# Optimization experiments

Measured on AMD Instinct MI355X. Metric: run time of the kernel, lower is better.

The kernel has to match this reference:

```python
import jax, jax.numpy as jnp
import numpy as np

B, H, S, D = 1, 16, 4096, 64


def setup_inputs() -> dict:
    key = jax.random.key(0)
    kq, kk, kv = jax.random.split(key, 3)
    Q = jax.random.normal(kq, (B, H, S, D), dtype=jnp.float32)
    K = jax.random.normal(kk, (B, H, S, D), dtype=jnp.float32)
    V = jax.random.normal(kv, (B, H, S, D), dtype=jnp.float32)
    # causal mask, broadcast over batch/heads: True = attend
    mask = jnp.tril(jnp.ones((S, S), dtype=bool))[None, None, :, :]
    return {"Q": Q, "K": K, "V": V, "mask": mask}


def reference(Q, K, V, mask):
    d_k = Q.shape[-1]
    scale = 1.0 / jnp.sqrt(jnp.asarray(d_k, dtype=Q.dtype))
    # [..., q, k] scores; mask==False positions set to -inf before softmax
    scores = jnp.einsum('...qd,...kd->...qk', Q, K) * scale
    scores = jnp.where(mask, scores, jnp.asarray(-jnp.inf, dtype=scores.dtype))
    attn = jax.nn.softmax(scores, axis=-1)
    return jnp.einsum('...qk,...kd->...qd', attn, V)
```

## Files before the change

### kernel.cpp

```cpp
#include <hip/hip_runtime.h>
#include <hip/hip_bf16.h>

typedef __attribute__((ext_vector_type(8))) short short8;
typedef __attribute__((ext_vector_type(4))) short s4v;
typedef __attribute__((ext_vector_type(4))) int   int4v;
typedef __attribute__((ext_vector_type(4))) float floatx4;

#define MFMA16(A,B,C) __builtin_amdgcn_mfma_f32_16x16x32_bf16(A,B,C,0,0,0)

__device__ __forceinline__ short bf16bits(float x) {
    __hip_bfloat16 h = __float2bfloat16(x);
    return *(short*)&h;
}
__device__ __forceinline__ short8 cvt8(const float* p) {
    floatx4 a = *(const floatx4*)p;
    floatx4 b = *(const floatx4*)(p + 4);
    short8 r;
    r[0]=bf16bits(a.x); r[1]=bf16bits(a.y); r[2]=bf16bits(a.z); r[3]=bf16bits(a.w);
    r[4]=bf16bits(b.x); r[5]=bf16bits(b.y); r[6]=bf16bits(b.z); r[7]=bf16bits(b.w);
    return r;
}
__device__ __forceinline__ short8 cvt8s(const float* p) {
    constexpr float SCL2 = 0.125f * 1.44269504088896f;
    floatx4 a = *(const floatx4*)p;
    floatx4 b = *(const floatx4*)(p + 4);
    a *= SCL2; b *= SCL2;
    short8 r;
    r[0]=bf16bits(a.x); r[1]=bf16bits(a.y); r[2]=bf16bits(a.z); r[3]=bf16bits(a.w);
    r[4]=bf16bits(b.x); r[5]=bf16bits(b.y); r[6]=bf16bits(b.z); r[7]=bf16bits(b.w);
    return r;
}
__device__ __forceinline__ int pk2(float lo, float hi) {
    int r;
    asm("v_cvt_pk_bf16_f32 %0, %1, %2" : "=v"(r) : "v"(lo), "v"(hi));
    return r;
}

__global__ __launch_bounds__(256) void prep(const float* __restrict__ V,
                                            short* __restrict__ VT,
                                            const float* __restrict__ K,
                                            short* __restrict__ K16, int doK)
{
    __shared__ short tile[64 * 65];
    const int t  = threadIdx.x;
    const int h  = blockIdx.x >> 6;
    const int s0 = (blockIdx.x & 63) << 6;
    const float* src = V + ((size_t)h * 4096 + s0) * 64;
    const int r = t >> 4, dq = (t & 15) * 4;
#pragma unroll
    for (int pass = 0; pass < 4; ++pass) {
        const int s = pass * 16 + r;
        floatx4 f = *(const floatx4*)(src + s * 64 + dq);
        short* w = tile + s * 65 + dq;
        w[0] = bf16bits(f.x); w[1] = bf16bits(f.y);
        w[2] = bf16bits(f.z); w[3] = bf16bits(f.w);
    }
    __syncthreads();
    const int d = t >> 2, sc = (t & 3) * 16;
    short8 a, b;
#pragma unroll
    for (int j = 0; j < 8; ++j) a[j] = tile[(sc + j) * 65 + d];
#pragma unroll
    for (int j = 0; j < 8; ++j) b[j] = tile[(sc + 8 + j) * 65 + d];
    short* dst = VT + ((size_t)h * 64 + d) * 4096 + s0 + sc;
    *(short8*)dst       = a;
    *(short8*)(dst + 8) = b;
    if (doK) {
        const size_t base = (size_t)blockIdx.x * 4096 + (size_t)t * 16;
        *(short8*)(K16 + base)     = cvt8(K + base);
        *(short8*)(K16 + base + 8) = cvt8(K + base + 8);
    }
}

__global__ __attribute__((amdgpu_waves_per_eu(4, 4))) __launch_bounds__(256)
void attn_split(const float* __restrict__ Qg, const short* __restrict__ K16g,
                const short* __restrict__ VTg, float* __restrict__ Og,
                float* __restrict__ partO, float* __restrict__ partL)
{
    constexpr int S = 4096, D = 64;

    __shared__ __align__(16) short lK[8192];
    __shared__ __align__(16) short lV[8192];

    const int tid = threadIdx.x;
    const int wv  = tid >> 6;
    const int ln  = tid & 63;
    const int ll  = ln & 15;
    const int qd  = ln >> 4;
    const int qhalf = wv & 1;
    const int khalf = wv >> 1;

    const int bid = blockIdx.x;
    const int h = bid / 95;
    const int u = bid % 95;
    int qblk, ks, ke, slot;
    if (u < 62) {
        qblk = 63 - (u >> 1);
        const int part = u & 1;
        const int T = qblk + 1, Th = T >> 1;
        ks = part ? Th : 0;
        ke = part ? T : Th;
        slot = (h * 31 + (qblk - 33)) * 2 + part;
    } else {
        qblk = 94 - u;
        ks = 0; ke = qblk + 1;
        slot = -1;
    }
    const int qb   = qblk << 6;
    const int qrow = qb + (qhalf << 5);

    const float* Qh  = Qg  + (size_t)h * S * D;
    const short* K16 = K16g + (size_t)h * S * D;
    const short* Vt  = VTg + (size_t)h * 64 * S;

    short8 qA0, qA1, qB0, qB1;
    {
        const float* qp = Qh + (qrow + ll) * D + qd * 8;
        qA0 = cvt8s(qp);       qA1 = cvt8s(qp + 32);
        const float* qp2 = qp + 16 * D;
        qB0 = cvt8s(qp2);      qB1 = cvt8s(qp2 + 32);
    }

    floatx4 oA[4], oB[4], olA, olB;
#pragma unroll
    for (int dt = 0; dt < 4; ++dt) { oA[dt] = (floatx4){0.f,0.f,0.f,0.f}; oB[dt] = oA[dt]; }
    olA = (floatx4){0.f,0.f,0.f,0.f};
    olB = olA;

    short8 ones;
#pragma unroll
    for (int j = 0; j < 8; ++j) ones[j] = (short)0x3F80;

    const int kkey = tid >> 3, kd8 = tid & 7;
    const int koct = kd8 & 3;
    short* kdst = lK + ((kkey >> 4) * 2 + (kd8 >> 2)) * 512
                     + ((((kkey & 15) | (koct << 4)) ^ (koct * 5)) * 8);
    const short* ksrc6 = K16 + kkey * 64 + kd8 * 8;
    const int vd = tid >> 2, voct = tid & 3;
    short* vdst = lV + (vd >> 4) * 512
                     + ((((vd & 15) | (voct << 4)) ^ (voct * 5)) * 8);
    const short* vsrc = Vt + (size_t)vd * S + voct * 8;
    const int rblk = ((ll | (qd << 4)) ^ (qd * 5));

    const int wv_end = qrow + 32;

    auto mkpf = [&](floatx4 sc0, floatx4 sc1, int qgrp, int kvh) -> short8 {
        float p0[4], p1[4];
#pragma unroll
        for (int r = 0; r < 4; ++r) { p0[r] = exp2f(sc0[r]); p1[r] = exp2f(sc1[r]); }
        if (kvh + 31 > qgrp) {
            const int qg = qgrp + ll;
            const int k0 = kvh + qd * 4, k1 = k0 + 16;
#pragma unroll
            for (int r = 0; r < 4; ++r) {
                if (k0 + r > qg) p0[r] = 0.f;
                if (k1 + r > qg) p1[r] = 0.f;
            }
        }
        int w0 = pk2(p0[0], p0[1]);
        int w1 = pk2(p0[2], p0[3]);
        int w2 = pk2(p1[0], p1[1]);
        int w3 = pk2(p1[2], p1[3]);
        asm("v_permlane32_swap_b32 %0, %1" : "+v"(w0), "+v"(w2));
        asm("v_permlane32_swap_b32 %0, %1" : "+v"(w1), "+v"(w3));
        asm("v_permlane16_swap_b32 %0, %1" : "+v"(w0), "+v"(w2));
        asm("v_permlane16_swap_b32 %0, %1" : "+v"(w1), "+v"(w3));
        int4v pv = {w0, w1, w2, w3};
        return *(short8*)&pv;
    };

    short8 kp0 = *(const short8*)(ksrc6 + ks * 64 * 64);
    short8 kp1 = *(const short8*)(ksrc6 + (ks * 64 + 32) * 64);
    short8 vp0 = *(const short8*)(vsrc + ks * 64);
    short8 vp1 = *(const short8*)(vsrc + ks * 64 + 32);

    int bo = 0;
    for (int t = ks; t <= ke; ++t) {
        __syncthreads();
        if (t < ke) {
            *(short8*)(kdst + bo)        = kp0;
            *(short8*)(kdst + bo + 2048) = kp1;
            *(short8*)(vdst + bo)        = vp0;
            *(short8*)(vdst + bo + 2048) = vp1;
            if (t + 1 < ke) {
                const int nk = (t + 1) << 6;
                kp0 = *(const short8*)(ksrc6 + (size_t)nk * 64);
                kp1 = *(const short8*)(ksrc6 + (size_t)(nk + 32) * 64);
                vp0 = *(const short8*)(vsrc + nk);
                vp1 = *(const short8*)(vsrc + nk + 32);
            }
        }
        if (t > ks) {
            const int kv  = (t - 1) << 6;
            const int kvw = kv + (khalf << 5);
            if (kvw < wv_end) {
                const int ro = (bo ^ 4096) + (khalf << 11);
                const short* Kb = lK + ro;
                const short* Vb = lV + ro;
                floatx4 zz = (floatx4){0.f,0.f,0.f,0.f};
                floatx4 sA0=zz, sA1=zz, sB0=zz, sB1=zz;
                short8 kf;
                __builtin_amdgcn_s_setprio(1);
                kf = ((const short8*)(Kb +    0))[rblk]; sA0 = MFMA16(kf, qA0, sA0); sB0 = MFMA16(kf, qB0, sB0);
                kf = ((const short8*)(Kb +  512))[rblk]; sA0 = MFMA16(kf, qA1, sA0); sB0 = MFMA16(kf, qB1, sB0);
                kf = ((const short8*)(Kb + 1024))[rblk]; sA1 = MFMA16(kf, qA0, sA1); sB1 = MFMA16(kf, qB0, sB1);
                kf = ((const short8*)(Kb + 1536))[rblk]; sA1 = MFMA16(kf, qA1, sA1); sB1 = MFMA16(kf, qB1, sB1);
                __builtin_amdgcn_s_setprio(0);

                short8 pfA = mkpf(sA0, sA1, qrow,      kvw);
                short8 pfB = mkpf(sB0, sB1, qrow + 16, kvw);
                __builtin_amdgcn_s_setprio(1);
#pragma unroll
                for (int dt = 0; dt < 4; ++dt) {
                    short8 vf = ((const short8*)(Vb + dt * 512))[rblk];
                    oA[dt] = MFMA16(pfA, vf, oA[dt]);
                    oB[dt] = MFMA16(pfB, vf, oB[dt]);
                }
                olA = MFMA16(pfA, ones, olA);
                olB = MFMA16(pfB, ones, olB);
                __builtin_amdgcn_s_setprio(0);
            }
        }
        bo ^= 4096;
    }

    __syncthreads();
    float* sAod = (float*)lK;
    float* sBod = (float*)lV;
    const int mbase = ((qhalf << 6) + ln) * 20;
    if (khalf == 1) {
#pragma unroll
        for (int dt = 0; dt < 4; ++dt)
#pragma unroll
            for (int r = 0; r < 4; ++r) {
                sAod[mbase + dt * 4 + r] = oA[dt][r];
                sBod[mbase + dt * 4 + r] = oB[dt][r];
            }
#pragma unroll
        for (int r = 0; r < 4; ++r) {
            sAod[mbase + 16 + r] = olA[r];
            sBod[mbase + 16 + r] = olB[r];
        }
    }
    __syncthreads();
    if (khalf == 0) {
#pragma unroll
        for (int dt = 0; dt < 4; ++dt)
#pragma unroll
            for (int r = 0; r < 4; ++r) {
                oA[dt][r] += sAod[mbase + dt * 4 + r];
                oB[dt][r] += sBod[mbase + dt * 4 + r];
            }
#pragma unroll
        for (int r = 0; r < 4; ++r) {
            olA[r] += sAod[mbase + 16 + r];
            olB[r] += sBod[mbase + 16 + r];
        }
        if (slot < 0) {
#pragma unroll
            for (int r = 0; r < 4; ++r) {
                const float rl = 1.f / fmaxf(olA[r], 1e-37f);
                const int q = qrow + qd * 4 + r;
                float* op = Og + ((size_t)h * S + q) * D + ll;
#pragma unroll
                for (int dt = 0; dt < 4; ++dt)
                    op[dt * 16] = oA[dt][r] * rl;
            }
#pragma unroll
            for (int r = 0; r < 4; ++r) {
                const float rl = 1.f / fmaxf(olB[r], 1e-37f);
                const int q = qrow + 16 + qd * 4 + r;
                float* op = Og + ((size_t)h * S + q) * D + ll;
#pragma unroll
                for (int dt = 0; dt < 4; ++dt)
                    op[dt * 16] = oB[dt][r] * rl;
            }
        } else {
            float* po = partO + (size_t)slot * 4096;
            float* pl = partL + (size_t)slot * 64;
#pragma unroll
            for (int r = 0; r < 4; ++r) {
                const int row = (qhalf << 5) + qd * 4 + r;
                float* op = po + row * 64 + ll;
#pragma unroll
                for (int dt = 0; dt < 4; ++dt)
                    op[dt * 16] = oA[dt][r];
                if (ll == 0) pl[row] = olA[r];
            }
#pragma unroll
            for (int r = 0; r < 4; ++r) {
                const int row = (qhalf << 5) + 16 + qd * 4 + r;
                float* op = po + row * 64 + ll;
#pragma unroll
                for (int dt = 0; dt < 4; ++dt)
                    op[dt * 16] = oB[dt][r];
                if (ll == 0) pl[row] = olB[r];
            }
        }
    }
}

__global__ __launch_bounds__(256) void merge_split(const float* __restrict__ pO,
                                                   const float* __restrict__ pL,
                                                   float* __restrict__ Og)
{
    const int bid = blockIdx.x;
    const int h  = bid / 31;
    const int qb = (33 + bid % 31) << 6;
    const size_t b0 = (size_t)(bid * 2) * 4096;
    const int t = threadIdx.x;
#pragma unroll
    for (int k = 0; k < 4; ++k) {
        const int idx = t * 4 + k * 1024;
        const int row = idx >> 6;
        floatx4 a = *(const floatx4*)(pO + b0 + idx);
        floatx4 b = *(const floatx4*)(pO + b0 + 4096 + idx);
        const float l = pL[bid * 128 + row] + pL[bid * 128 + 64 + row];
        const float rl = 1.f / fmaxf(l, 1e-37f);
        floatx4 o;
        o.x = (a.x + b.x) * rl; o.y = (a.y + b.y) * rl;
        o.z = (a.z + b.z) * rl; o.w = (a.w + b.w) * rl;
        *(floatx4*)(Og + ((size_t)h * 4096 + qb + row) * 64 + (idx & 63)) = o;
    }
}

template<bool KB16>
__global__ __attribute__((amdgpu_waves_per_eu(4, 4))) __launch_bounds__(256)
void attn_fast(const float* __restrict__ Qg, const float* __restrict__ Kg,
               const short* __restrict__ K16g, const short* __restrict__ VTg,
               float* __restrict__ Og)
{
    constexpr int S = 4096, D = 64;
    __shared__ __align__(16) short lK[8192];
    __shared__ __align__(16) short lV[8192];
    const int tid = threadIdx.x;
    const int wv  = tid >> 6;
    const int ln  = tid & 63;
    const int ll  = ln & 15;
    const int qd  = ln >> 4;
    const int qhalf = wv & 1;
    const int khalf = wv >> 1;
    const int c = blockIdx.x & 255;
    const int s = blockIdx.x >> 8;
    const int h = c & 15;
    const int x = c >> 4;
    const int qblk = (s == 0) ? (63 - x) : (s == 1) ? (32 + x) : (s == 2) ? (31 - x) : x;
    const int qb   = qblk << 6;
    const int qrow = qb + (qhalf << 5);
    const float* Qh  = Qg  + (size_t)h * S * D;
    const float* Kf  = Kg  + (size_t)h * S * D;
    const short* K16 = K16g + (size_t)h * S * D;
    const short* Vt  = VTg + (size_t)h * 64 * S;
    short8 qA0, qA1, qB0, qB1;
    {
        const float* qp = Qh + (qrow + ll) * D + qd * 8;
        qA0 = cvt8s(qp);       qA1 = cvt8s(qp + 32);
        const float* qp2 = qp + 16 * D;
        qB0 = cvt8s(qp2);      qB1 = cvt8s(qp2 + 32);
    }
    floatx4 oA[4], oB[4], olA, olB;
#pragma unroll
    for (int dt = 0; dt < 4; ++dt) { oA[dt] = (floatx4){0.f,0.f,0.f,0.f}; oB[dt] = oA[dt]; }
    olA = (floatx4){0.f,0.f,0.f,0.f};
    olB = olA;
    short8 ones;
#pragma unroll
    for (int j = 0; j < 8; ++j) ones[j] = (short)0x3F80;
    const int kkey = tid >> 3, kd8 = tid & 7;
    const int koct = kd8 & 3;
    short* kdst = lK + ((kkey >> 4) * 2 + (kd8 >> 2)) * 512
                     + ((((kkey & 15) | (koct << 4)) ^ (koct * 5)) * 8);
    const float* ksrcf = Kf  + kkey * 64 + kd8 * 8;
    const short* ksrc6 = K16 + kkey * 64 + kd8 * 8;
    const int vd = tid >> 2, voct = tid & 3;
    short* vdst = lV + (vd >> 4) * 512
                     + ((((vd & 15) | (voct << 4)) ^ (voct * 5)) * 8);
    const short* vsrc = Vt + (size_t)vd * S + voct * 8;
    const int rblk = ((ll | (qd << 4)) ^ (qd * 5));
    const int kv_end = qb + 64;
    const int wv_end = qrow + 32;
    auto ldK = [&](int kv) -> short8 {
        return KB16 ? *(const short8*)(ksrc6 + kv * 64) : cvt8(ksrcf + kv * 64);
    };
    auto mkpf = [&](floatx4 sc0, floatx4 sc1, int qgrp, int kvh) -> short8 {
        float p0[4], p1[4];
#pragma unroll
        for (int r = 0; r < 4; ++r) { p0[r] = exp2f(sc0[r]); p1[r] = exp2f(sc1[r]); }
        if (kvh + 31 > qgrp) {
            const int qg = qgrp + ll;
            const int k0 = kvh + qd * 4, k1 = k0 + 16;
#pragma unroll
            for (int r = 0; r < 4; ++r) {
                if (k0 + r > qg) p0[r] = 0.f;
                if (k1 + r > qg) p1[r] = 0.f;
            }
        }
        int w0 = pk2(p0[0], p0[1]);
        int w1 = pk2(p0[2], p0[3]);
        int w2 = pk2(p1[0], p1[1]);
        int w3 = pk2(p1[2], p1[3]);
        asm("v_permlane32_swap_b32 %0, %1" : "+v"(w0), "+v"(w2));
        asm("v_permlane32_swap_b32 %0, %1" : "+v"(w1), "+v"(w3));
        asm("v_permlane16_swap_b32 %0, %1" : "+v"(w0), "+v"(w2));
        asm("v_permlane16_swap_b32 %0, %1" : "+v"(w1), "+v"(w3));
        int4v pv = {w0, w1, w2, w3};
        return *(short8*)&pv;
    };
    short8 kp0 = ldK(0),  kp1 = ldK(32);
    short8 vp0 = *(const short8*)(vsrc);
    short8 vp1 = *(const short8*)(vsrc + 32);
    const int ntiles = kv_end >> 6;
    int bo = 0;
    for (int t = 0; t <= ntiles; ++t) {
        __syncthreads();
        if (t < ntiles) {
            *(short8*)(kdst + bo)        = kp0;
            *(short8*)(kdst + bo + 2048) = kp1;
            *(short8*)(vdst + bo)        = vp0;
            *(short8*)(vdst + bo + 2048) = vp1;
            const int nk = (t + 1) << 6;
            if (nk < kv_end) {
                kp0 = ldK(nk);
                kp1 = ldK(nk + 32);
                vp0 = *(const short8*)(vsrc + nk);
                vp1 = *(const short8*)(vsrc + nk + 32);
            }
        }
        if (t > 0) {
            const int kv  = (t - 1) << 6;
            const int kvw = kv + (khalf << 5);
            if (kvw < wv_end) {
                const int ro = (bo ^ 4096) + (khalf << 11);
                const short* Kb = lK + ro;
                const short* Vb = lV + ro;
                floatx4 zz = (floatx4){0.f,0.f,0.f,0.f};
                floatx4 sA0=zz, sA1=zz, sB0=zz, sB1=zz;
                short8 kf;
                __builtin_amdgcn_s_setprio(1);
                kf = ((const short8*)(Kb +    0))[rblk]; sA0 = MFMA16(kf, qA0, sA0); sB0 = MFMA16(kf, qB0, sB0);
                kf = ((const short8*)(Kb +  512))[rblk]; sA0 = MFMA16(kf, qA1, sA0); sB0 = MFMA16(kf, qB1, sB0);
                kf = ((const short8*)(Kb + 1024))[rblk]; sA1 = MFMA16(kf, qA0, sA1); sB1 = MFMA16(kf, qB0, sB1);
                kf = ((const short8*)(Kb + 1536))[rblk]; sA1 = MFMA16(kf, qA1, sA1); sB1 = MFMA16(kf, qB1, sB1);
                __builtin_amdgcn_s_setprio(0);
                short8 pfA = mkpf(sA0, sA1, qrow,      kvw);
                short8 pfB = mkpf(sB0, sB1, qrow + 16, kvw);
                __builtin_amdgcn_s_setprio(1);
#pragma unroll
                for (int dt = 0; dt < 4; ++dt) {
                    short8 vf = ((const short8*)(Vb + dt * 512))[rblk];
                    oA[dt] = MFMA16(pfA, vf, oA[dt]);
                    oB[dt] = MFMA16(pfB, vf, oB[dt]);
                }
                olA = MFMA16(pfA, ones, olA);
                olB = MFMA16(pfB, ones, olB);
                __builtin_amdgcn_s_setprio(0);
            }
        }
        bo ^= 4096;
    }
    __syncthreads();
    float* sAod = (float*)lK;
    float* sBod = (float*)lV;
    const int mbase = ((qhalf << 6) + ln) * 20;
    if (khalf == 1) {
#pragma unroll
        for (int dt = 0; dt < 4; ++dt)
#pragma unroll
            for (int r = 0; r < 4; ++r) {
                sAod[mbase + dt * 4 + r] = oA[dt][r];
                sBod[mbase + dt * 4 + r] = oB[dt][r];
            }
#pragma unroll
        for (int r = 0; r < 4; ++r) {
            sAod[mbase + 16 + r] = olA[r];
            sBod[mbase + 16 + r] = olB[r];
        }
    }
    __syncthreads();
    if (khalf == 0) {
#pragma unroll
        for (int dt = 0; dt < 4; ++dt)
#pragma unroll
            for (int r = 0; r < 4; ++r) {
                oA[dt][r] += sAod[mbase + dt * 4 + r];
                oB[dt][r] += sBod[mbase + dt * 4 + r];
            }
#pragma unroll
        for (int r = 0; r < 4; ++r) {
            olA[r] += sAod[mbase + 16 + r];
            olB[r] += sBod[mbase + 16 + r];
        }
#pragma unroll
        for (int r = 0; r < 4; ++r) {
            const float rl = 1.f / fmaxf(olA[r], 1e-37f);
            const int q = qrow + qd * 4 + r;
            float* op = Og + ((size_t)h * S + q) * D + ll;
#pragma unroll
            for (int dt = 0; dt < 4; ++dt)
                op[dt * 16] = oA[dt][r] * rl;
        }
#pragma unroll
        for (int r = 0; r < 4; ++r) {
            const float rl = 1.f / fmaxf(olB[r], 1e-37f);
            const int q = qrow + 16 + qd * 4 + r;
            float* op = Og + ((size_t)h * S + q) * D + ll;
#pragma unroll
            for (int dt = 0; dt < 4; ++dt)
                op[dt * 16] = oB[dt][r] * rl;
        }
    }
}

__global__ __launch_bounds__(256, 4)
void attn_legacy(const float* __restrict__ Qg, const float* __restrict__ Kg,
                 const float* __restrict__ Vg, float* __restrict__ Og)
{
    constexpr int S = 4096, D = 64;
    constexpr float SCL2 = 0.125f * 1.44269504088896f;
    constexpr float NEG  = -1.0e30f;
    __shared__ __align__(16) short lK[2048];
    __shared__ __align__(16) short lV[2048];
    __shared__ __align__(16) short lP[2048];
    const int tid = threadIdx.x, wv = tid >> 6, ln = tid & 63, ll = ln & 15, qd = ln >> 4;
    const int bid = blockIdx.x, h = bid & 15, qblk = 63 - (bid >> 4), qb = qblk << 6;
    const float* Qh = Qg + (size_t)h * S * D;
    const float* Kh = Kg + (size_t)h * S * D;
    const float* Vh = Vg + (size_t)h * S * D;
    const int qrow = qb + wv * 16;
    short8 qf0, qf1;
    { const float* qp = Qh + (qrow + ll) * D + qd * 8; qf0 = cvt8(qp); qf1 = cvt8(qp + 32); }
    floatx4 o[4]; float mi[4], li[4];
#pragma unroll
    for (int dt = 0; dt < 4; ++dt) o[dt] = (floatx4){0.f,0.f,0.f,0.f};
#pragma unroll
    for (int r = 0; r < 4; ++r) { mi[r] = NEG; li[r] = 0.f; }
    const int k_st = tid >> 3, dbase = (tid & 7) * 8;
    const int sq = (dbase >> 3) & 3, sks = dbase >> 5;
    const int kw_slot = (((k_st >> 4) * 2 + sks) * 64)
                      + (((sq << 4) | (k_st & 15)) ^ (sq | (sks << 2)));
    const int kr0 = ln ^ qd, kr1 = ln ^ (qd | 4), vbit3 = (ln >> 3) & 1;
    const int kv_end = qb + 64, wv_end = qrow + 16;
    for (int kv = 0; kv < kv_end; kv += 32) {
        __syncthreads();
        {
            short8 kval = cvt8(Kh + (kv + k_st) * D + dbase);
            ((short8*)lK)[kw_slot] = kval;
            short8 vval = cvt8(Vh + (kv + k_st) * D + dbase);
            const int vq = (k_st >> 3) << 4, vj = k_st & 7;
#pragma unroll
            for (int i = 0; i < 8; ++i) {
                int d = dbase + i, dt = d >> 4, l2 = d & 15;
                int lp = (vq | l2) ^ (((l2 >> 3) & 1) | (dt << 1));
                lV[dt * 512 + lp * 8 + vj] = vval[i];
            }
        }
        __syncthreads();
        if (kv < wv_end) {
            floatx4 sc0 = (floatx4){0.f,0.f,0.f,0.f}, sc1 = sc0; short8 kf;
            kf = ((const short8*)lK)[0*64+kr0]; sc0 = MFMA16(qf0, kf, sc0);
            kf = ((const short8*)lK)[1*64+kr1]; sc0 = MFMA16(qf1, kf, sc0);
            kf = ((const short8*)lK)[2*64+kr0]; sc1 = MFMA16(qf0, kf, sc1);
            kf = ((const short8*)lK)[3*64+kr1]; sc1 = MFMA16(qf1, kf, sc1);
            float p0[4], p1[4]; const int qg = qrow + qd * 4;
#pragma unroll
            for (int r = 0; r < 4; ++r) { p0[r] = sc0[r]*SCL2; p1[r] = sc1[r]*SCL2; }
            if (kv + 31 > qrow) {
                const int k0 = kv + ll, k1 = kv + 16 + ll;
#pragma unroll
                for (int r = 0; r < 4; ++r) {
                    if (k0 > qg + r) p0[r] = NEG;
                    if (k1 > qg + r) p1[r] = NEG;
                }
            }
#pragma unroll
            for (int r = 0; r < 4; ++r) {
                float mx = fmaxf(p0[r], p1[r]);
                mx = fmaxf(mx, __shfl_xor(mx,1)); mx = fmaxf(mx, __shfl_xor(mx,2));
                mx = fmaxf(mx, __shfl_xor(mx,4)); mx = fmaxf(mx, __shfl_xor(mx,8));
                const float nm = fmaxf(mi[r], mx);
                const float a = exp2f(mi[r] - nm); mi[r] = nm;
                p0[r] = exp2f(p0[r] - nm); p1[r] = exp2f(p1[r] - nm);
                float ps = p0[r] + p1[r];
                ps += __shfl_xor(ps,1); ps += __shfl_xor(ps,2);
                ps += __shfl_xor(ps,4); ps += __shfl_xor(ps,8);
                li[r] = li[r] * a + ps;
#pragma unroll
                for (int dt = 0; dt < 4; ++dt) o[dt][r] *= a;
            }
            {
                const int pbase = wv * 512 + (ll & 7);
                const int dl0 = ((ll >> 3) << 4) + qd * 4;
#pragma unroll
                for (int r = 0; r < 4; ++r) {
                    lP[pbase + (dl0 + r) * 8]      = bf16bits(p0[r]);
                    lP[pbase + (dl0 + 32 + r) * 8] = bf16bits(p1[r]);
                }
            }
            __threadfence_block();
            short8 pf = ((const short8*)lP)[wv * 64 + ln];
#pragma unroll
            for (int dt = 0; dt < 4; ++dt) {
                short8 vf = ((const short8*)lV)[dt * 64 + (ln ^ (vbit3 | (dt << 1)))];
                o[dt] = MFMA16(pf, vf, o[dt]);
            }
        }
    }
#pragma unroll
    for (int r = 0; r < 4; ++r) {
        const float rl = 1.f / fmaxf(li[r], 1e-30f);
        const int q = qrow + qd * 4 + r;
        float* op = Og + ((size_t)h * S + q) * D + ll;
#pragma unroll
        for (int dt = 0; dt < 4; ++dt) op[dt * 16] = o[dt][r] * rl;
    }
}

extern "C" void kernel_launch(void* const* d_in, const int* in_sizes, int n_in,
                              void* d_out, int out_size, void* d_ws, size_t ws_size,
                              hipStream_t stream) {
    const float* Q = (const float*)d_in[0];
    const float* K = (const float*)d_in[1];
    const float* V = (const float*)d_in[2];
    float* O = (float*)d_out;
    const size_t elems  = (size_t)16 * 4096 * 64;
    const size_t oneBuf = elems * sizeof(short);
    const size_t partOB = (size_t)992 * 4096 * sizeof(float);
    const size_t partLB = (size_t)992 * 64 * sizeof(float);
    if (ws_size >= 2 * oneBuf + partOB + partLB) {
        short* VT  = (short*)d_ws;
        short* K16 = (short*)d_ws + elems;
        float* pO  = (float*)((char*)d_ws + 2 * oneBuf);
        float* pL  = pO + (size_t)992 * 4096;
        prep<<<dim3(1024), dim3(256), 0, stream>>>(V, VT, K, K16, 1);
        attn_split<<<dim3(1520), dim3(256), 0, stream>>>(Q, K16, VT, O, pO, pL);
        merge_split<<<dim3(496), dim3(256), 0, stream>>>(pO, pL, O);
    } else if (ws_size >= 2 * oneBuf) {
        short* VT  = (short*)d_ws;
        short* K16 = (short*)d_ws + elems;
        prep<<<dim3(1024), dim3(256), 0, stream>>>(V, VT, K, K16, 1);
        attn_fast<true><<<dim3(1024), dim3(256), 0, stream>>>(Q, K, K16, VT, O);
    } else if (ws_size >= oneBuf) {
        short* VT = (short*)d_ws;
        prep<<<dim3(1024), dim3(256), 0, stream>>>(V, VT, K, VT, 0);
        attn_fast<false><<<dim3(1024), dim3(256), 0, stream>>>(Q, K, nullptr, VT, O);
    } else {
        attn_legacy<<<dim3(1024), dim3(256), 0, stream>>>(Q, K, V, O);
    }
}
```

Baseline: 203.5 us.

## Rebalance causal split-K work into paired equal-length block segments

```diff
diff --git a/kernel.cpp b/kernel.cpp
--- a/kernel.cpp
+++ b/kernel.cpp
@@ -72,10 +72,10 @@
     }
 }
 
-__global__ __attribute__((amdgpu_waves_per_eu(4, 4))) __launch_bounds__(256)
-void attn_split(const float* __restrict__ Qg, const short* __restrict__ K16g,
-                const short* __restrict__ VTg, float* __restrict__ Og,
-                float* __restrict__ partO, float* __restrict__ partL)
+__global__ __attribute__((amdgpu_waves_per_eu(4, 8))) __launch_bounds__(256)
+void attn_pair(const float* __restrict__ Qg, const short* __restrict__ K16g,
+               const short* __restrict__ VTg, float* __restrict__ Og,
+               float* __restrict__ partO, float* __restrict__ partL)
 {
     constexpr int S = 4096, D = 64;
 
@@ -90,46 +90,14 @@
     const int qhalf = wv & 1;
     const int khalf = wv >> 1;
 
-    const int bid = blockIdx.x;
-    const int h = bid / 95;
-    const int u = bid % 95;
-    int qblk, ks, ke, slot;
-    if (u < 62) {
-        qblk = 63 - (u >> 1);
-        const int part = u & 1;
-        const int T = qblk + 1, Th = T >> 1;
-        ks = part ? Th : 0;
-        ke = part ? T : Th;
-        slot = (h * 31 + (qblk - 33)) * 2 + part;
-    } else {
-        qblk = 94 - u;
-        ks = 0; ke = qblk + 1;
-        slot = -1;
-    }
-    const int qb   = qblk << 6;
-    const int qrow = qb + (qhalf << 5);
+    const int bid  = blockIdx.x;
+    const int h    = bid & 15;
+    const int x    = (bid >> 4) & 31;
+    const int role = bid >> 9;
 
     const float* Qh  = Qg  + (size_t)h * S * D;
     const short* K16 = K16g + (size_t)h * S * D;
     const short* Vt  = VTg + (size_t)h * 64 * S;
-
-    short8 qA0, qA1, qB0, qB1;
-    {
-        const float* qp = Qh + (qrow + ll) * D + qd * 8;
-        qA0 = cvt8s(qp);       qA1 = cvt8s(qp + 32);
-        const float* qp2 = qp + 16 * D;
-        qB0 = cvt8s(qp2);      qB1 = cvt8s(qp2 + 32);
-    }
-
-    floatx4 oA[4], oB[4], olA, olB;
-#pragma unroll
-    for (int dt = 0; dt < 4; ++dt) { oA[dt] = (floatx4){0.f,0.f,0.f,0.f}; oB[dt] = oA[dt]; }
-    olA = (floatx4){0.f,0.f,0.f,0.f};
-    olB = olA;
-
-    short8 ones;
-#pragma unroll
-    for (int j = 0; j < 8; ++j) ones[j] = (short)0x3F80;
 
     const int kkey = tid >> 3, kd8 = tid & 7;
     const int koct = kd8 & 3;
@@ -142,172 +110,204 @@
     const short* vsrc = Vt + (size_t)vd * S + voct * 8;
     const int rblk = ((ll | (qd << 4)) ^ (qd * 5));
 
-    const int wv_end = qrow + 32;
-
-    auto mkpf = [&](floatx4 sc0, floatx4 sc1, int qgrp, int kvh) -> short8 {
-        float p0[4], p1[4];
-#pragma unroll
-        for (int r = 0; r < 4; ++r) { p0[r] = exp2f(sc0[r]); p1[r] = exp2f(sc1[r]); }
-        if (kvh + 31 > qgrp) {
-            const int qg = qgrp + ll;
-            const int k0 = kvh + qd * 4, k1 = k0 + 16;
+    short8 ones;
+#pragma unroll
+    for (int j = 0; j < 8; ++j) ones[j] = (short)0x3F80;
+
+    auto runSeg = [&](int qblk, int ks, int ke, int slot) {
+        const int qb     = qblk << 6;
+        const int qrow   = qb + (qhalf << 5);
+        const int wv_end = qrow + 32;
+
+        short8 qA0, qA1, qB0, qB1;
+        {
+            const float* qp = Qh + (qrow + ll) * D + qd * 8;
+            qA0 = cvt8s(qp);       qA1 = cvt8s(qp + 32);
+            const float* qp2 = qp + 16 * D;
+            qB0 = cvt8s(qp2);      qB1 = cvt8s(qp2 + 32);
+        }
+
+        floatx4 oA[4], oB[4], olA, olB;
+#pragma unroll
+        for (int dt = 0; dt < 4; ++dt) { oA[dt] = (floatx4){0.f,0.f,0.f,0.f}; oB[dt] = oA[dt]; }
+        olA = (floatx4){0.f,0.f,0.f,0.f};
+        olB = olA;
+
+        auto mkpf = [&](floatx4 sc0, floatx4 sc1, int qgrp, int kvh) -> short8 {
+            float p0[4], p1[4];
+#pragma unroll
+            for (int r = 0; r < 4; ++r) { p0[r] = exp2f(sc0[r]); p1[r] = exp2f(sc1[r]); }
+            if (kvh + 31 > qgrp) {
+                const int qg = qgrp + ll;
+                const int k0 = kvh + qd * 4, k1 = k0 + 16;
+#pragma unroll
+                for (int r = 0; r < 4; ++r) {
+                    if (k0 + r > qg) p0[r] = 0.f;
+                    if (k1 + r > qg) p1[r] = 0.f;
+                }
+            }
+            int w0 = pk2(p0[0], p0[1]);
+            int w1 = pk2(p0[2], p0[3]);
+            int w2 = pk2(p1[0], p1[1]);
+            int w3 = pk2(p1[2], p1[3]);
+            asm("v_permlane32_swap_b32 %0, %1" : "+v"(w0), "+v"(w2));
+            asm("v_permlane32_swap_b32 %0, %1" : "+v"(w1), "+v"(w3));
+            asm("v_permlane16_swap_b32 %0, %1" : "+v"(w0), "+v"(w2));
+            asm("v_permlane16_swap_b32 %0, %1" : "+v"(w1), "+v"(w3));
+            int4v pv = {w0, w1, w2, w3};
+            return *(short8*)&pv;
+        };
+
+        short8 kp0 = *(const short8*)(ksrc6 + (size_t)(ks * 64) * 64);
+        short8 kp1 = *(const short8*)(ksrc6 + (size_t)(ks * 64 + 32) * 64);
+        short8 vp0 = *(const short8*)(vsrc + ks * 64);
+        short8 vp1 = *(const short8*)(vsrc + ks * 64 + 32);
+
+        int bo = 0;
+        for (int t = ks; t <= ke; ++t) {
+            __syncthreads();
+            if (t < ke) {
+                *(short8*)(kdst + bo)        = kp0;
+                *(short8*)(kdst + bo + 2048) = kp1;
+                *(short8*)(vdst + bo)        = vp0;
+                *(short8*)(vdst + bo + 2048) = vp1;
+                if (t + 1 < ke) {
+                    const int nk = (t + 1) << 6;
+                    kp0 = *(const short8*)(ksrc6 + (size_t)nk * 64);
+                    kp1 = *(const short8*)(ksrc6 + (size_t)(nk + 32) * 64);
+                    vp0 = *(const short8*)(vsrc + nk);
+                    vp1 = *(const short8*)(vsrc + nk + 32);
+                }
+            }
+            if (t > ks) {
+                const int kv  = (t - 1) << 6;
+                const int kvw = kv + (khalf << 5);
+                if (kvw < wv_end) {
+                    const int ro = (bo ^ 4096) + (khalf << 11);
+                    const short* Kb = lK + ro;
+                    const short* Vb = lV + ro;
+                    floatx4 zz = (floatx4){0.f,0.f,0.f,0.f};
+                    floatx4 sA0=zz, sA1=zz, sB0=zz, sB1=zz;
+                    short8 kf;
+                    __builtin_amdgcn_s_setprio(1);
+                    kf = ((const short8*)(Kb +    0))[rblk]; sA0 = MFMA16(kf, qA0, sA0); sB0 = MFMA16(kf, qB0, sB0);
+                    kf = ((const short8*)(Kb +  512))[rblk]; sA0 = MFMA16(kf, qA1, sA0); sB0 = MFMA16(kf, qB1, sB0);
+                    kf = ((const short8*)(Kb + 1024))[rblk]; sA1 = MFMA16(kf, qA0, sA1); sB1 = MFMA16(kf, qB0, sB1);
+                    kf = ((const short8*)(Kb + 1536))[rblk]; sA1 = MFMA16(kf, qA1, sA1); sB1 = MFMA16(kf, qB1, sB1);
+                    __builtin_amdgcn_s_setprio(0);
+
+                    short8 pfA = mkpf(sA0, sA1, qrow,      kvw);
+                    short8 pfB = mkpf(sB0, sB1, qrow + 16, kvw);
+                    __builtin_amdgcn_s_setprio(1);
+#pragma unroll
+                    for (int dt = 0; dt < 4; ++dt) {
+                        short8 vf = ((const short8*)(Vb + dt * 512))[rblk];
+                        oA[dt] = MFMA16(pfA, vf, oA[dt]);
+                        oB[dt] = MFMA16(pfB, vf, oB[dt]);
+                    }
+                    olA = MFMA16(pfA, ones, olA);
+                    olB = MFMA16(pfB, ones, olB);
+                    __builtin_amdgcn_s_setprio(0);
+                }
+            }
+            bo ^= 4096;
+        }
+
+        __syncthreads();
+        float* sAod = (float*)lK;
+        float* sBod = (float*)lV;
+        const int mbase = ((qhalf << 6) + ln) * 20;
+        if (khalf == 1) {
+#pragma unroll
+            for (int dt = 0; dt < 4; ++dt)
+#pragma unroll
+                for (int r = 0; r < 4; ++r) {
+                    sAod[mbase + dt * 4 + r] = oA[dt][r];
+                    sBod[mbase + dt * 4 + r] = oB[dt][r];
+                }
 #pragma unroll
             for (int r = 0; r < 4; ++r) {
-                if (k0 + r > qg) p0[r] = 0.f;
-                if (k1 + r > qg) p1[r] = 0.f;
-            }
-        }
-        int w0 = pk2(p0[0], p0[1]);
-        int w1 = pk2(p0[2], p0[3]);
-        int w2 = pk2(p1[0], p1[1]);
-        int w3 = pk2(p1[2], p1[3]);
-        asm("v_permlane32_swap_b32 %0, %1" : "+v"(w0), "+v"(w2));
-        asm("v_permlane32_swap_b32 %0, %1" : "+v"(w1), "+v"(w3));
-        asm("v_permlane16_swap_b32 %0, %1" : "+v"(w0), "+v"(w2));
-        asm("v_permlane16_swap_b32 %0, %1" : "+v"(w1), "+v"(w3));
-        int4v pv = {w0, w1, w2, w3};
-        return *(short8*)&pv;
+                sAod[mbase + 16 + r] = olA[r];
+                sBod[mbase + 16 + r] = olB[r];
+            }
+        }
+        __syncthreads();
+        if (khalf == 0) {
+#pragma unroll
+            for (int dt = 0; dt < 4; ++dt)
+#pragma unroll
+                for (int r = 0; r < 4; ++r) {
+                    oA[dt][r] += sAod[mbase + dt * 4 + r];
+                    oB[dt][r] += sBod[mbase + dt * 4 + r];
+                }
+#pragma unroll
+            for (int r = 0; r < 4; ++r) {
+                olA[r] += sAod[mbase + 16 + r];
+                olB[r] += sBod[mbase + 16 + r];
+            }
+            if (slot < 0) {
+#pragma unroll
+                for (int r = 0; r < 4; ++r) {
+                    const float rl = 1.f / fmaxf(olA[r], 1e-37f);
+                    const int q = qrow + qd * 4 + r;
+                    float* op = Og + ((size_t)h * S + q) * D + ll;
+#pragma unroll
+                    for (int dt = 0; dt < 4; ++dt)
+                        op[dt * 16] = oA[dt][r] * rl;
+                }
+#pragma unroll
+                for (int r = 0; r < 4; ++r) {
+                    const float rl = 1.f / fmaxf(olB[r], 1e-37f);
+                    const int q = qrow + 16 + qd * 4 + r;
+                    float* op = Og + ((size_t)h * S + q) * D + ll;
+#pragma unroll
+                    for (int dt = 0; dt < 4; ++dt)
+                        op[dt * 16] = oB[dt][r] * rl;
+                }
+            } else {
+                float* po = partO + (size_t)slot * 4096;
+                float* pl = partL + (size_t)slot * 64;
+#pragma unroll
+                for (int r = 0; r < 4; ++r) {
+                    const int row = (qhalf << 5) + qd * 4 + r;
+                    float* op = po + row * 64 + ll;
+#pragma unroll
+                    for (int dt = 0; dt < 4; ++dt)
+                        op[dt * 16] = oA[dt][r];
+                    if (ll == 0) pl[row] = olA[r];
+                }
+#pragma unroll
+                for (int r = 0; r < 4; ++r) {
+                    const int row = (qhalf << 5) + 16 + qd * 4 + r;
+                    float* op = po + row * 64 + ll;
+#pragma unroll
+                    for (int dt = 0; dt < 4; ++dt)
+                        op[dt * 16] = oB[dt][r];
+                    if (ll == 0) pl[row] = olB[r];
+                }
+            }
+        }
     };
 
-    short8 kp0 = *(const short8*)(ksrc6 + ks * 64 * 64);
-    short8 kp1 = *(const short8*)(ksrc6 + (ks * 64 + 32) * 64);
-    short8 vp0 = *(const short8*)(vsrc + ks * 64);
-    short8 vp1 = *(const short8*)(vsrc + ks * 64 + 32);
-
-    int bo = 0;
-    for (int t = ks; t <= ke; ++t) {
-        __syncthreads();
-        if (t < ke) {
-            *(short8*)(kdst + bo)        = kp0;
-            *(short8*)(kdst + bo + 2048) = kp1;
-            *(short8*)(vdst + bo)        = vp0;
-            *(short8*)(vdst + bo + 2048) = vp1;
-            if (t + 1 < ke) {
-                const int nk = (t + 1) << 6;
-                kp0 = *(const short8*)(ksrc6 + (size_t)nk * 64);
-                kp1 = *(const short8*)(ksrc6 + (size_t)(nk + 32) * 64);
-                vp0 = *(const short8*)(vsrc + nk);
-                vp1 = *(const short8*)(vsrc + nk + 32);
-            }
-        }
-        if (t > ks) {
-            const int kv  = (t - 1) << 6;
-            const int kvw = kv + (khalf << 5);
-            if (kvw < wv_end) {
-                const int ro = (bo ^ 4096) + (khalf << 11);
-                const short* Kb = lK + ro;
-                const short* Vb = lV + ro;
-                floatx4 zz = (floatx4){0.f,0.f,0.f,0.f};
-                floatx4 sA0=zz, sA1=zz, sB0=zz, sB1=zz;
-                short8 kf;
-                __builtin_amdgcn_s_setprio(1);
-                kf = ((const short8*)(Kb +    0))[rblk]; sA0 = MFMA16(kf, qA0, sA0); sB0 = MFMA16(kf, qB0, sB0);
-                kf = ((const short8*)(Kb +  512))[rblk]; sA0 = MFMA16(kf, qA1, sA0); sB0 = MFMA16(kf, qB1, sB0);
-                kf = ((const short8*)(Kb + 1024))[rblk]; sA1 = MFMA16(kf, qA0, sA1); sB1 = MFMA16(kf, qB0, sB1);
-                kf = ((const short8*)(Kb + 1536))[rblk]; sA1 = MFMA16(kf, qA1, sA1); sB1 = MFMA16(kf, qB1, sB1);
-                __builtin_amdgcn_s_setprio(0);
-
-                short8 pfA = mkpf(sA0, sA1, qrow,      kvw);
-                short8 pfB = mkpf(sB0, sB1, qrow + 16, kvw);
-                __builtin_amdgcn_s_setprio(1);
-#pragma unroll
-                for (int dt = 0; dt < 4; ++dt) {
-                    short8 vf = ((const short8*)(Vb + dt * 512))[rblk];
-                    oA[dt] = MFMA16(pfA, vf, oA[dt]);
-                    oB[dt] = MFMA16(pfB, vf, oB[dt]);
-                }
-                olA = MFMA16(pfA, ones, olA);
-                olB = MFMA16(pfB, ones, olB);
-                __builtin_amdgcn_s_setprio(0);
-            }
-        }
-        bo ^= 4096;
-    }
-
-    __syncthreads();
-    float* sAod = (float*)lK;
-    float* sBod = (float*)lV;
-    const int mbase = ((qhalf << 6) + ln) * 20;
-    if (khalf == 1) {
-#pragma unroll
-        for (int dt = 0; dt < 4; ++dt)
-#pragma unroll
-            for (int r = 0; r < 4; ++r) {
-                sAod[mbase + dt * 4 + r] = oA[dt][r];
-                sBod[mbase + dt * 4 + r] = oB[dt][r];
-            }
-#pragma unroll
-        for (int r = 0; r < 4; ++r) {
-            sAod[mbase + 16 + r] = olA[r];
-            sBod[mbase + 16 + r] = olB[r];
-        }
-    }
-    __syncthreads();
-    if (khalf == 0) {
-#pragma unroll
-        for (int dt = 0; dt < 4; ++dt)
-#pragma unroll
-            for (int r = 0; r < 4; ++r) {
-                oA[dt][r] += sAod[mbase + dt * 4 + r];
-                oB[dt][r] += sBod[mbase + dt * 4 + r];
-            }
-#pragma unroll
-        for (int r = 0; r < 4; ++r) {
-            olA[r] += sAod[mbase + 16 + r];
-            olB[r] += sBod[mbase + 16 + r];
-        }
-        if (slot < 0) {
-#pragma unroll
-            for (int r = 0; r < 4; ++r) {
-                const float rl = 1.f / fmaxf(olA[r], 1e-37f);
-                const int q = qrow + qd * 4 + r;
-                float* op = Og + ((size_t)h * S + q) * D + ll;
-#pragma unroll
-                for (int dt = 0; dt < 4; ++dt)
-                    op[dt * 16] = oA[dt][r] * rl;
-            }
-#pragma unroll
-            for (int r = 0; r < 4; ++r) {
-                const float rl = 1.f / fmaxf(olB[r], 1e-37f);
-                const int q = qrow + 16 + qd * 4 + r;
-                float* op = Og + ((size_t)h * S + q) * D + ll;
-#pragma unroll
-                for (int dt = 0; dt < 4; ++dt)
-                    op[dt * 16] = oB[dt][r] * rl;
-            }
-        } else {
-            float* po = partO + (size_t)slot * 4096;
-            float* pl = partL + (size_t)slot * 64;
-#pragma unroll
-            for (int r = 0; r < 4; ++r) {
-                const int row = (qhalf << 5) + qd * 4 + r;
-                float* op = po + row * 64 + ll;
-#pragma unroll
-                for (int dt = 0; dt < 4; ++dt)
-                    op[dt * 16] = oA[dt][r];
-                if (ll == 0) pl[row] = olA[r];
-            }
-#pragma unroll
-            for (int r = 0; r < 4; ++r) {
-                const int row = (qhalf << 5) + 16 + qd * 4 + r;
-                float* op = po + row * 64 + ll;
-#pragma unroll
-                for (int dt = 0; dt < 4; ++dt)
-                    op[dt * 16] = oB[dt][r];
-                if (ll == 0) pl[row] = olB[r];
-            }
-        }
-    }
-}
-
-__global__ __launch_bounds__(256) void merge_split(const float* __restrict__ pO,
-                                                   const float* __restrict__ pL,
-                                                   float* __restrict__ Og)
+    const int slotBase = (h * 32 + x) * 2;
+    if (role == 0) {
+        runSeg(63 - x, 0, 33, slotBase);
+    } else {
+        runSeg(63 - x, 33, 64 - x, slotBase + 1);
+        runSeg(x, 0, x + 1, -1);
+    }
+}
+
+__global__ __launch_bounds__(256) void merge_pair(const float* __restrict__ pO,
+                                                  const float* __restrict__ pL,
+                                                  float* __restrict__ Og)
 {
     const int bid = blockIdx.x;
-    const int h  = bid / 31;
-    const int qb = (33 + bid % 31) << 6;
-    const size_t b0 = (size_t)(bid * 2) * 4096;
+    const int h  = bid & 15;
+    const int x  = bid >> 4;
+    const int qb = (63 - x) << 6;
+    const int sb = (h * 32 + x) * 2;
+    const size_t b0 = (size_t)sb * 4096;
     const int t = threadIdx.x;
 #pragma unroll
     for (int k = 0; k < 4; ++k) {
@@ -315,7 +315,7 @@
         const int row = idx >> 6;
         floatx4 a = *(const floatx4*)(pO + b0 + idx);
         floatx4 b = *(const floatx4*)(pO + b0 + 4096 + idx);
-        const float l = pL[bid * 128 + row] + pL[bid * 128 + 64 + row];
+        const float l = pL[sb * 64 + row] + pL[sb * 64 + 64 + row];
         const float rl = 1.f / fmaxf(l, 1e-37f);
         floatx4 o;
         o.x = (a.x + b.x) * rl; o.y = (a.y + b.y) * rl;
@@ -325,7 +325,7 @@
 }
 
 template<bool KB16>
-__global__ __attribute__((amdgpu_waves_per_eu(4, 4))) __launch_bounds__(256)
+__global__ __attribute__((amdgpu_waves_per_eu(4, 8))) __launch_bounds__(256)
 void attn_fast(const float* __restrict__ Qg, const float* __restrict__ Kg,
                const short* __restrict__ K16g, const short* __restrict__ VTg,
                float* __restrict__ Og)
@@ -624,16 +624,16 @@
     float* O = (float*)d_out;
     const size_t elems  = (size_t)16 * 4096 * 64;
     const size_t oneBuf = elems * sizeof(short);
-    const size_t partOB = (size_t)992 * 4096 * sizeof(float);
-    const size_t partLB = (size_t)992 * 64 * sizeof(float);
+    const size_t partOB = (size_t)1024 * 4096 * sizeof(float);
+    const size_t partLB = (size_t)1024 * 64 * sizeof(float);
     if (ws_size >= 2 * oneBuf + partOB + partLB) {
         short* VT  = (short*)d_ws;
         short* K16 = (short*)d_ws + elems;
         float* pO  = (float*)((char*)d_ws + 2 * oneBuf);
-        float* pL  = pO + (size_t)992 * 4096;
+        float* pL  = pO + (size_t)1024 * 4096;
         prep<<<dim3(1024), dim3(256), 0, stream>>>(V, VT, K, K16, 1);
-        attn_split<<<dim3(1520), dim3(256), 0, stream>>>(Q, K16, VT, O, pO, pL);
-        merge_split<<<dim3(496), dim3(256), 0, stream>>>(pO, pL, O);
+        attn_pair<<<dim3(1024), dim3(256), 0, stream>>>(Q, K16, VT, O, pO, pL);
+        merge_pair<<<dim3(512), dim3(256), 0, stream>>>(pO, pL, O);
     } else if (ws_size >= 2 * oneBuf) {
         short* VT  = (short*)d_ws;
         short* K16 = (short*)d_ws + elems;
```

Result: faster. 194.6 us (-4.4%).
